# Kernel tuning notes

Measured on AMD Instinct MI355X. Metric: run time of the kernel, lower is better.

## Reference

```python
import jax, jax.numpy as jnp
import numpy as np

B, LQ, LK = 16, 256, 256
DQ = DK = DV = H = 256


def setup_inputs() -> dict:
    key = jax.random.key(0)
    ks = jax.random.split(key, 7)
    queries = jax.random.normal(ks[0], (B, LQ, DQ), dtype=jnp.float32)
    keys = jax.random.normal(ks[1], (B, LK, DK), dtype=jnp.float32)
    values = jax.random.normal(ks[2], (B, LK, DV), dtype=jnp.float32)
    valid_lens = jax.random.randint(ks[3], (B,), 1, LK + 1).astype(jnp.int32)
    W_q = jax.random.normal(ks[4], (DQ, H), dtype=jnp.float32) / np.sqrt(DQ)
    W_k = jax.random.normal(ks[5], (DK, H), dtype=jnp.float32) / np.sqrt(DK)
    w_v = jax.random.normal(ks[6], (H,), dtype=jnp.float32) / np.sqrt(H)
    return {"queries": queries, "keys": keys, "values": values,
            "valid_lens": valid_lens, "W_q": W_q, "W_k": W_k, "w_v": w_v}


def reference(queries, keys, values, valid_lens, W_q, W_k, w_v):
    # Project queries and keys to the hidden size (no bias)
    q = jnp.einsum('bqd,dh->bqh', queries, W_q)          # (B, Lq, H)
    k = jnp.einsum('bkd,dh->bkh', keys, W_k)             # (B, Lk, H)
    # Broadcast-add, tanh, then contract with w_v -> scores (B, Lq, Lk)
    features = jnp.tanh(q[:, :, None, :] + k[:, None, :, :])  # (B, Lq, Lk, H)
    scores = jnp.einsum('bqkh,h->bqk', features, w_v)
    # Masked softmax over last axis: positions >= valid_len get -1e6
    mask = jnp.arange(scores.shape[-1]) < valid_lens[:, None, None]  # (B,1,Lk) bcast
    scores = jnp.where(mask, scores, jnp.float32(-1e6))
    attn = jax.nn.softmax(scores, axis=-1)
    # Dropout is identity at inference (training=False)
    return jnp.einsum('bqk,bkv->bqv', attn, values)      # (B, Lq, Dv)
```

## Files before the change

kernel.cpp:

```cpp
#include <hip/hip_runtime.h>

using bf16x8 = __attribute__((ext_vector_type(8))) __bf16;
using f32x4  = __attribute__((ext_vector_type(4))) float;
using f32x2  = __attribute__((ext_vector_type(2))) float;
using us8    = __attribute__((ext_vector_type(8))) unsigned short;

#define TWO_LOG2E 2.8853900817779268f
#define LOG2E 1.4426950408889634f

__device__ __forceinline__ unsigned short f2bf(float x) {
  unsigned int u = __float_as_uint(x);
  u = (u + 0x7fffu + ((u >> 16) & 1u)) >> 16;
  return (unsigned short)u;
}
__device__ __forceinline__ float bf2f(unsigned short h) {
  return __uint_as_float(((unsigned int)h) << 16);
}

__global__ __launch_bounds__(256) void tcast_kernel(
    const float* __restrict__ Wq, const float* __restrict__ Wk,
    const float* __restrict__ vals, const float* __restrict__ wv,
    const int* __restrict__ vlens,
    unsigned short* __restrict__ wt_hi, unsigned short* __restrict__ wt_lo,
    unsigned short* __restrict__ vt_hi, unsigned short* __restrict__ vt_lo,
    float* __restrict__ wv2, float* __restrict__ Wsum,
    unsigned short* __restrict__ jobs, int* __restrict__ ctr) {
  if (blockIdx.x == 0) {
    int t = threadIdx.x;
    wv2[t] = -2.0f * wv[t];
    if (t < 64) {
      float s = wv[t] + wv[t + 64] + wv[t + 128] + wv[t + 192];
#pragma unroll
      for (int off = 1; off < 64; off <<= 1) s += __shfl_xor(s, off, 64);
      if (t == 0) Wsum[0] = s;
    }
    if (t == 0) {
      ctr[0] = 0;
      int n = 0;
      for (int lvl = 4; lvl >= 1; --lvl)
        for (int b = 0; b < 16; ++b) {
          int kt = (vlens[b] + 63) >> 6;
          if (kt == lvl)
            for (int q = 0; q < 32; ++q)
              jobs[n++] = (unsigned short)((b << 5) | q);
        }
    }
  }
  __shared__ float tile[32][33];
  int m = blockIdx.x >> 6;
  int ts = blockIdx.x & 63;
  int R0 = (ts >> 3) << 5, C0 = (ts & 7) << 5;
  const float* src = (m == 0) ? Wq : (m == 1) ? Wk : (vals + ((m - 2) << 16));
  int r = threadIdx.x >> 3, c4 = (threadIdx.x & 7) << 2;
  float4 v = *(const float4*)(src + (R0 + r) * 256 + C0 + c4);
  tile[r][c4] = v.x; tile[r][c4 + 1] = v.y; tile[r][c4 + 2] = v.z; tile[r][c4 + 3] = v.w;
  __syncthreads();
  float o0 = tile[c4 + 0][r], o1 = tile[c4 + 1][r];
  float o2 = tile[c4 + 2][r], o3 = tile[c4 + 3][r];
  unsigned short h0 = f2bf(o0), h1 = f2bf(o1), h2 = f2bf(o2), h3 = f2bf(o3);
  int base = ((m < 2) ? (m << 16) : ((m - 2) << 16)) + (C0 + r) * 256 + R0 + c4;
  unsigned short* dh = (m < 2) ? wt_hi : vt_hi;
  unsigned short* dl = (m < 2) ? wt_lo : vt_lo;
  *(ushort4*)(dh + base) = make_ushort4(h0, h1, h2, h3);
  *(ushort4*)(dl + base) = make_ushort4(f2bf(o0 - bf2f(h0)), f2bf(o1 - bf2f(h1)),
                                        f2bf(o2 - bf2f(h2)), f2bf(o3 - bf2f(h3)));
}

__global__ __launch_bounds__(256, 4) void proj_kernel(
    const float* __restrict__ q, const float* __restrict__ kk,
    const unsigned short* __restrict__ w_hi, const unsigned short* __restrict__ w_lo,
    const int* __restrict__ vlens, float* __restrict__ Rq, float* __restrict__ RkT) {
  int wave = threadIdx.x >> 6, lane = threadIdx.x & 63;
  int mt = (blockIdx.x << 1) + (wave & 1);
  int m0 = mt << 4;
  int g = mt >> 8;
  int r = lane & 15, qd = lane >> 4;
  int nbase = (blockIdx.y << 6) + ((wave >> 1) << 5);
  if (g) {
    int bb = (m0 >> 8) & 15;
    if ((m0 & 255) >= vlens[bb]) {
      f32x4 z = {0.f, 0.f, 0.f, 0.f};
      int kloc = (m0 & 255) + qd * 4;
#pragma unroll
      for (int tI = 0; tI < 2; ++tI)
        *(f32x4*)(RkT + (bb << 16) + (nbase + (tI << 4) + r) * 256 + kloc) = z;
      return;
    }
  }
  int row = m0 + r;
  const float* A = (g == 0) ? (q + row * 256) : (kk + (row - 4096) * 256);
  int boff0 = (g << 16) + (nbase + r) * 256 + qd * 8;
  int boff1 = boff0 + (16 << 8);
  f32x4 acc0 = {0.f, 0.f, 0.f, 0.f}, acc1 = {0.f, 0.f, 0.f, 0.f};
#pragma unroll
  for (int kh = 0; kh < 2; ++kh) {
    bf16x8 ah[4], al[4];
#pragma unroll
    for (int s = 0; s < 4; ++s) {
      const float* p = A + qd * 8 + (kh * 4 + s) * 32;
      float4 f0 = *(const float4*)p;
      float4 f1 = *(const float4*)(p + 4);
      float fv[8] = {f0.x, f0.y, f0.z, f0.w, f1.x, f1.y, f1.z, f1.w};
#pragma unroll
      for (int j = 0; j < 8; ++j) {
        __bf16 h = (__bf16)fv[j];
        ah[s][j] = h;
        al[s][j] = (__bf16)(fv[j] - (float)h);
      }
    }
#pragma unroll
    for (int s = 0; s < 4; ++s) {
      int off = (kh * 4 + s) * 32;
      bf16x8 bh0 = *(const bf16x8*)(w_hi + boff0 + off);
      bf16x8 bl0 = *(const bf16x8*)(w_lo + boff0 + off);
      acc0 = __builtin_amdgcn_mfma_f32_16x16x32_bf16(ah[s], bh0, acc0, 0, 0, 0);
      acc0 = __builtin_amdgcn_mfma_f32_16x16x32_bf16(ah[s], bl0, acc0, 0, 0, 0);
      acc0 = __builtin_amdgcn_mfma_f32_16x16x32_bf16(al[s], bh0, acc0, 0, 0, 0);
      bf16x8 bh1 = *(const bf16x8*)(w_hi + boff1 + off);
      bf16x8 bl1 = *(const bf16x8*)(w_lo + boff1 + off);
      acc1 = __builtin_amdgcn_mfma_f32_16x16x32_bf16(ah[s], bh1, acc1, 0, 0, 0);
      acc1 = __builtin_amdgcn_mfma_f32_16x16x32_bf16(ah[s], bl1, acc1, 0, 0, 0);
      acc1 = __builtin_amdgcn_mfma_f32_16x16x32_bf16(al[s], bh1, acc1, 0, 0, 0);
    }
  }
#pragma unroll
  for (int tI = 0; tI < 2; ++tI) {
    f32x4 acc = tI ? acc1 : acc0;
    int n0 = nbase + (tI << 4);
    f32x4 ex;
#pragma unroll
    for (int i = 0; i < 4; ++i) {
      float l = acc[i] * TWO_LOG2E;
      l = fminf(fmaxf(l, -27.f), 27.f);
      ex[i] = __builtin_amdgcn_exp2f(l);
    }
    if (g == 0) {
#pragma unroll
      for (int i = 0; i < 4; ++i)
        Rq[(m0 + qd * 4 + i) * 256 + n0 + r] = ex[i];
    } else {
      int b = (m0 >> 8) & 15;
      int kloc = (m0 & 255) + qd * 4;
      *(f32x4*)(RkT + (b << 16) + (n0 + r) * 256 + kloc) = ex;
    }
  }
}

__global__ __launch_bounds__(512) void sav3_kernel(
    const float* __restrict__ Rq, const float* __restrict__ RkT,
    const float* __restrict__ wv2, const float* __restrict__ Wsum,
    const int* __restrict__ vlens, const unsigned short* __restrict__ jobs,
    int* __restrict__ ctr,
    const unsigned short* __restrict__ vhi, const unsigned short* __restrict__ vlo,
    float* __restrict__ out) {
  __shared__ __align__(16) float kT[256 * 68];
  __shared__ __align__(16) float rqs[8 * 260];
  __shared__ __align__(16) float scs[8 * 260];
  __shared__ __align__(16) unsigned short athi[16 * 264];
  __shared__ float wv2s[256];
  __shared__ int s_item;
  const int t = threadIdx.x;
  const int w = t >> 6, lane = t & 63;
  const float wsum = Wsum[0];

  if (t < 256) wv2s[t] = wv2[t];
  for (int i = t; i < 8 * 264; i += 512) athi[8 * 264 + i] = 0;

  for (;;) {
    __syncthreads();
    if (t == 0) s_item = atomicAdd(ctr, 1);
    __syncthreads();
    const int jid = s_item;
    if (jid >= 512) return;
    const int jw = jobs[jid];
    const int b = jw >> 5, q0 = (jw & 31) << 3;
    const int qrow = (b << 8) + q0;
    const int vl = vlens[b];
    const int ktiles = (vl + 63) >> 6;

    {
      int row = t >> 6, c = lane << 2;
      *(float4*)(rqs + row * 260 + c) = *(const float4*)(Rq + (qrow + row) * 256 + c);
    }
    for (int kt = 0; kt < ktiles; ++kt) {
      const int k0 = kt << 6;
      __syncthreads();
      {
        int h0 = t >> 2, kc = (t & 3) << 4;
#pragma unroll
        for (int p = 0; p < 2; ++p) {
          int h = h0 + (p << 7);
          const float* gk = RkT + (b << 16) + h * 256 + k0 + kc;
          *(float4*)(kT + h * 68 + kc)      = *(const float4*)gk;
          *(float4*)(kT + h * 68 + kc + 4)  = *(const float4*)(gk + 4);
          *(float4*)(kT + h * 68 + kc + 8)  = *(const float4*)(gk + 8);
          *(float4*)(kT + h * 68 + kc + 12) = *(const float4*)(gk + 12);
        }
      }
      __syncthreads();
      float a = 0.f;
#pragma unroll 4
      for (int h = 0; h < 256; ++h) {
        float qa = rqs[w * 260 + h];
        float wm = wv2s[h];
        float rk = kT[h * 68 + lane];
        float d = __builtin_fmaf(rk, qa, 1.0f);
        a = __builtin_fmaf(__builtin_amdgcn_rcpf(d), wm, a);
      }
      scs[w * 260 + k0 + lane] = a + wsum;
    }
    __syncthreads();

    {
      int c0 = lane << 2;
      float4 x = *(const float4*)(scs + w * 260 + c0);
      float p[4] = {x.x, x.y, x.z, x.w};
#pragma unroll
      for (int i = 0; i < 4; ++i)
        if (c0 + i >= vl) p[i] = -1e6f;
      float mx = fmaxf(fmaxf(p[0], p[1]), fmaxf(p[2], p[3]));
#pragma unroll
      for (int off = 1; off < 64; off <<= 1) mx = fmaxf(mx, __shfl_xor(mx, off, 64));
      float sm = 0.f;
#pragma unroll
      for (int i = 0; i < 4; ++i) {
        p[i] = __builtin_amdgcn_exp2f((p[i] - mx) * LOG2E);
        sm += p[i];
      }
#pragma unroll
      for (int off = 1; off < 64; off <<= 1) sm += __shfl_xor(sm, off, 64);
      float rs = __builtin_amdgcn_rcpf(sm);
      ushort4 vh;
      vh.x = f2bf(p[0] * rs); vh.y = f2bf(p[1] * rs);
      vh.z = f2bf(p[2] * rs); vh.w = f2bf(p[3] * rs);
      *(ushort4*)(athi + w * 264 + c0) = vh;
    }
    __syncthreads();

    {
      const int r = lane & 15, qd = lane >> 4;
      const int smax = (vl + 31) >> 5;
      const int nb = w << 5;
      const int boff = (b << 16) + (nb + r) * 256 + qd * 8;
      f32x4 acc0 = {0.f, 0.f, 0.f, 0.f}, acc1 = {0.f, 0.f, 0.f, 0.f};
      for (int s = 0; s < smax; ++s) {
        bf16x8 pa = *(const bf16x8*)(athi + r * 264 + qd * 8 + s * 32);
        bf16x8 bh0 = *(const bf16x8*)(vhi + boff + s * 32);
        bf16x8 bl0 = *(const bf16x8*)(vlo + boff + s * 32);
        acc0 = __builtin_amdgcn_mfma_f32_16x16x32_bf16(pa, bh0, acc0, 0, 0, 0);
        acc0 = __builtin_amdgcn_mfma_f32_16x16x32_bf16(pa, bl0, acc0, 0, 0, 0);
        bf16x8 bh1 = *(const bf16x8*)(vhi + boff + (16 << 8) + s * 32);
        bf16x8 bl1 = *(const bf16x8*)(vlo + boff + (16 << 8) + s * 32);
        acc1 = __builtin_amdgcn_mfma_f32_16x16x32_bf16(pa, bh1, acc1, 0, 0, 0);
        acc1 = __builtin_amdgcn_mfma_f32_16x16x32_bf16(pa, bl1, acc1, 0, 0, 0);
      }
      if (qd < 2) {
#pragma unroll
        for (int i = 0; i < 4; ++i) {
          out[(b << 16) + (q0 + qd * 4 + i) * 256 + nb + r]      = acc0[i];
          out[(b << 16) + (q0 + qd * 4 + i) * 256 + nb + 16 + r] = acc1[i];
        }
      }
    }
  }
}

extern "C" void kernel_launch(void* const* d_in, const int* in_sizes, int n_in,
                              void* d_out, int out_size, void* d_ws, size_t ws_size,
                              hipStream_t stream) {
  const float* queries = (const float*)d_in[0];
  const float* keys    = (const float*)d_in[1];
  const float* values  = (const float*)d_in[2];
  const int*   vlens   = (const int*)d_in[3];
  const float* Wq      = (const float*)d_in[4];
  const float* Wk      = (const float*)d_in[5];
  const float* wv      = (const float*)d_in[6];
  float* out = (float*)d_out;
  char* ws = (char*)d_ws;

  unsigned short* wt_hi = (unsigned short*)(ws + 0);
  unsigned short* wt_lo = (unsigned short*)(ws + 262144);
  unsigned short* vt_hi = (unsigned short*)(ws + 524288);
  unsigned short* vt_lo = (unsigned short*)(ws + 2621440);
  float*          Rq    = (float*)(ws + 4718592);
  float*          RkT   = (float*)(ws + 8912896);
  float*          wv2   = (float*)(ws + 13107200);
  float*          Wsum  = (float*)(ws + 13108224);
  unsigned short* jobs  = (unsigned short*)(ws + 13109248);
  int*            ctr   = (int*)(ws + 13110272);

  tcast_kernel<<<1152, 256, 0, stream>>>(Wq, Wk, values, wv, vlens,
                                         wt_hi, wt_lo, vt_hi, vt_lo, wv2, Wsum,
                                         jobs, ctr);
  proj_kernel<<<dim3(256, 4), 256, 0, stream>>>(queries, keys, wt_hi, wt_lo,
                                                vlens, Rq, RkT);
  sav3_kernel<<<256, 512, 0, stream>>>(Rq, RkT, wv2, Wsum, vlens, jobs, ctr,
                                       vt_hi, vt_lo, out);
}
```

Before: 146.0 us.

## Stage 128-key mega-tiles and compute two query rows per wave in score loop

The score kernel now loads 128 keys of the exp-transformed key projection into shared memory per barrier instead of 64, halving the number of load/sync rounds. Each wave handles two query rows for one 64-key half, so each key value read from LDS is reused twice, and query and weight values are read as float4 vectors. The cost is a larger LDS footprint (about 135KB for kTm) and idle waves when the valid length leaves only one 64-key tile in the last mega-tile.

```diff
diff --git a/kernel.cpp b/kernel.cpp
--- a/kernel.cpp
+++ b/kernel.cpp
@@ -146,18 +146,18 @@
   }
 }
 
-__global__ __launch_bounds__(512) void sav3_kernel(
+__global__ __launch_bounds__(512) void sav5_kernel(
     const float* __restrict__ Rq, const float* __restrict__ RkT,
     const float* __restrict__ wv2, const float* __restrict__ Wsum,
     const int* __restrict__ vlens, const unsigned short* __restrict__ jobs,
     int* __restrict__ ctr,
     const unsigned short* __restrict__ vhi, const unsigned short* __restrict__ vlo,
     float* __restrict__ out) {
-  __shared__ __align__(16) float kT[256 * 68];
+  __shared__ __align__(16) float kTm[256 * 132];
   __shared__ __align__(16) float rqs[8 * 260];
-  __shared__ __align__(16) float scs[8 * 260];
+  __shared__ __align__(16) float scs[8 * 264];
   __shared__ __align__(16) unsigned short athi[16 * 264];
-  __shared__ float wv2s[256];
+  __shared__ __align__(16) float wv2s[256];
   __shared__ int s_item;
   const int t = threadIdx.x;
   const int w = t >> 6, lane = t & 63;
@@ -165,6 +165,10 @@
 
   if (t < 256) wv2s[t] = wv2[t];
   for (int i = t; i < 8 * 264; i += 512) athi[8 * 264 + i] = 0;
+
+  const int ql  = (w & 3) << 1;
+  const int ktl = w >> 2;
+  const int kloc = (ktl << 6) + lane;
 
   for (;;) {
     __syncthreads();
@@ -176,44 +180,60 @@
     const int b = jw >> 5, q0 = (jw & 31) << 3;
     const int qrow = (b << 8) + q0;
     const int vl = vlens[b];
-    const int ktiles = (vl + 63) >> 6;
+    const int kt64 = (vl + 63) >> 6;
+    const int nmega = (kt64 + 1) >> 1;
 
     {
       int row = t >> 6, c = lane << 2;
       *(float4*)(rqs + row * 260 + c) = *(const float4*)(Rq + (qrow + row) * 256 + c);
     }
-    for (int kt = 0; kt < ktiles; ++kt) {
-      const int k0 = kt << 6;
+
+    for (int m = 0; m < nmega; ++m) {
       __syncthreads();
       {
-        int h0 = t >> 2, kc = (t & 3) << 4;
-#pragma unroll
-        for (int p = 0; p < 2; ++p) {
-          int h = h0 + (p << 7);
-          const float* gk = RkT + (b << 16) + h * 256 + k0 + kc;
-          *(float4*)(kT + h * 68 + kc)      = *(const float4*)gk;
-          *(float4*)(kT + h * 68 + kc + 4)  = *(const float4*)(gk + 4);
-          *(float4*)(kT + h * 68 + kc + 8)  = *(const float4*)(gk + 8);
-          *(float4*)(kT + h * 68 + kc + 12) = *(const float4*)(gk + 12);
+        int hh = t >> 3, kc = (t & 7) << 4;
+#pragma unroll
+        for (int p = 0; p < 4; ++p) {
+          int h = (p << 6) + hh;
+          const float* gk = RkT + (b << 16) + h * 256 + (m << 7) + kc;
+          float* dst = kTm + h * 132 + kc;
+          *(float4*)(dst)      = *(const float4*)(gk);
+          *(float4*)(dst + 4)  = *(const float4*)(gk + 4);
+          *(float4*)(dst + 8)  = *(const float4*)(gk + 8);
+          *(float4*)(dst + 12) = *(const float4*)(gk + 12);
         }
       }
       __syncthreads();
-      float a = 0.f;
-#pragma unroll 4
-      for (int h = 0; h < 256; ++h) {
-        float qa = rqs[w * 260 + h];
-        float wm = wv2s[h];
-        float rk = kT[h * 68 + lane];
-        float d = __builtin_fmaf(rk, qa, 1.0f);
-        a = __builtin_fmaf(__builtin_amdgcn_rcpf(d), wm, a);
-      }
-      scs[w * 260 + k0 + lane] = a + wsum;
+      const int tiles = kt64 - (m << 1);
+      if (ktl < tiles) {
+        const float* kp = kTm + kloc;
+        const float* qa0 = rqs + ql * 260;
+        const float* qa1 = qa0 + 260;
+        float acc0 = 0.f, acc1 = 0.f;
+#pragma unroll 2
+        for (int h = 0; h < 256; h += 4) {
+          f32x4 wa = *(const f32x4*)(wv2s + h);
+          f32x4 a0 = *(const f32x4*)(qa0 + h);
+          f32x4 a1 = *(const f32x4*)(qa1 + h);
+#pragma unroll
+          for (int j = 0; j < 4; ++j) {
+            float rk = kp[(h + j) * 132];
+            float d0 = __builtin_fmaf(rk, a0[j], 1.0f);
+            float d1 = __builtin_fmaf(rk, a1[j], 1.0f);
+            acc0 = __builtin_fmaf(__builtin_amdgcn_rcpf(d0), wa[j], acc0);
+            acc1 = __builtin_fmaf(__builtin_amdgcn_rcpf(d1), wa[j], acc1);
+          }
+        }
+        const int kg = (m << 7) + kloc;
+        scs[ql * 264 + kg]       = acc0 + wsum;
+        scs[(ql + 1) * 264 + kg] = acc1 + wsum;
+      }
     }
     __syncthreads();
 
     {
       int c0 = lane << 2;
-      float4 x = *(const float4*)(scs + w * 260 + c0);
+      float4 x = *(const float4*)(scs + w * 264 + c0);
       float p[4] = {x.x, x.y, x.z, x.w};
 #pragma unroll
       for (int i = 0; i < 4; ++i)
@@ -294,6 +314,6 @@
                                          jobs, ctr);
   proj_kernel<<<dim3(256, 4), 256, 0, stream>>>(queries, keys, wt_hi, wt_lo,
                                                 vlens, Rq, RkT);
-  sav3_kernel<<<256, 512, 0, stream>>>(Rq, RkT, wv2, Wsum, vlens, jobs, ctr,
+  sav5_kernel<<<256, 512, 0, stream>>>(Rq, RkT, wv2, Wsum, vlens, jobs, ctr,
                                        vt_hi, vt_lo, out);
 }
```

After: 147.0 us. Within noise of the previous version (+0.7%).

## Store key projection row-major and split H across half-waves in score kernel

Applied to the files above, without the earlier changes.

The projection kernel now writes the exponentiated key projection row-major (k, h) instead of transposed. The score kernel tiles keys in 32-row chunks with a padded LDS stride. Each half-wave covers half of the hidden dimension with float4 reads and the two halves are combined by a cross-lane shuffle. Query rows and w_v are read straight from global memory instead of being staged in LDS. This cuts LDS use, finer key tiling trims wasted work past valid_len, and the grid doubles to 512 persistent blocks, at the cost of redundant global/L1 reads of the query rows and an extra shuffle per tile.

```diff
diff --git a/kernel.cpp b/kernel.cpp
--- a/kernel.cpp
+++ b/kernel.cpp
@@ -69,7 +69,7 @@
 __global__ __launch_bounds__(256, 4) void proj_kernel(
     const float* __restrict__ q, const float* __restrict__ kk,
     const unsigned short* __restrict__ w_hi, const unsigned short* __restrict__ w_lo,
-    const int* __restrict__ vlens, float* __restrict__ Rq, float* __restrict__ RkT) {
+    const int* __restrict__ vlens, float* __restrict__ Rq, float* __restrict__ Rk) {
   int wave = threadIdx.x >> 6, lane = threadIdx.x & 63;
   int mt = (blockIdx.x << 1) + (wave & 1);
   int m0 = mt << 4;
@@ -80,10 +80,10 @@
     int bb = (m0 >> 8) & 15;
     if ((m0 & 255) >= vlens[bb]) {
       f32x4 z = {0.f, 0.f, 0.f, 0.f};
-      int kloc = (m0 & 255) + qd * 4;
-#pragma unroll
-      for (int tI = 0; tI < 2; ++tI)
-        *(f32x4*)(RkT + (bb << 16) + (nbase + (tI << 4) + r) * 256 + kloc) = z;
+      int krow = m0 - 4096;
+#pragma unroll
+      for (int c = 0; c < 2; ++c)
+        *(f32x4*)(Rk + (krow + r) * 256 + nbase + qd * 8 + c * 4) = z;
       return;
     }
   }
@@ -139,32 +139,32 @@
       for (int i = 0; i < 4; ++i)
         Rq[(m0 + qd * 4 + i) * 256 + n0 + r] = ex[i];
     } else {
-      int b = (m0 >> 8) & 15;
-      int kloc = (m0 & 255) + qd * 4;
-      *(f32x4*)(RkT + (b << 16) + (n0 + r) * 256 + kloc) = ex;
-    }
-  }
-}
-
-__global__ __launch_bounds__(512) void sav3_kernel(
-    const float* __restrict__ Rq, const float* __restrict__ RkT,
+#pragma unroll
+      for (int i = 0; i < 4; ++i)
+        Rk[((m0 - 4096) + qd * 4 + i) * 256 + n0 + r] = ex[i];
+    }
+  }
+}
+
+__global__ __launch_bounds__(512) void sav6_kernel(
+    const float* __restrict__ Rq, const float* __restrict__ Rk,
     const float* __restrict__ wv2, const float* __restrict__ Wsum,
     const int* __restrict__ vlens, const unsigned short* __restrict__ jobs,
     int* __restrict__ ctr,
     const unsigned short* __restrict__ vhi, const unsigned short* __restrict__ vlo,
     float* __restrict__ out) {
-  __shared__ __align__(16) float kT[256 * 68];
-  __shared__ __align__(16) float rqs[8 * 260];
+  __shared__ __align__(16) float kS[32 * 257];
   __shared__ __align__(16) float scs[8 * 260];
   __shared__ __align__(16) unsigned short athi[16 * 264];
-  __shared__ float wv2s[256];
   __shared__ int s_item;
   const int t = threadIdx.x;
   const int w = t >> 6, lane = t & 63;
   const float wsum = Wsum[0];
 
-  if (t < 256) wv2s[t] = wv2[t];
   for (int i = t; i < 8 * 264; i += 512) athi[8 * 264 + i] = 0;
+
+  const int skrow = t & 31, schunk = t >> 5;
+  const int ck = lane & 31, chg = lane >> 5;
 
   for (;;) {
     __syncthreads();
@@ -176,38 +176,38 @@
     const int b = jw >> 5, q0 = (jw & 31) << 3;
     const int qrow = (b << 8) + q0;
     const int vl = vlens[b];
-    const int ktiles = (vl + 63) >> 6;
-
-    {
-      int row = t >> 6, c = lane << 2;
-      *(float4*)(rqs + row * 260 + c) = *(const float4*)(Rq + (qrow + row) * 256 + c);
-    }
-    for (int kt = 0; kt < ktiles; ++kt) {
-      const int k0 = kt << 6;
+    const int kt32 = (vl + 31) >> 5;
+
+    const float* qp = Rq + (qrow + w) * 256 + (chg << 7);
+    const float* wp = wv2 + (chg << 7);
+
+    for (int kt = 0; kt < kt32; ++kt) {
+      const int k0 = kt << 5;
       __syncthreads();
       {
-        int h0 = t >> 2, kc = (t & 3) << 4;
-#pragma unroll
-        for (int p = 0; p < 2; ++p) {
-          int h = h0 + (p << 7);
-          const float* gk = RkT + (b << 16) + h * 256 + k0 + kc;
-          *(float4*)(kT + h * 68 + kc)      = *(const float4*)gk;
-          *(float4*)(kT + h * 68 + kc + 4)  = *(const float4*)(gk + 4);
-          *(float4*)(kT + h * 68 + kc + 8)  = *(const float4*)(gk + 8);
-          *(float4*)(kT + h * 68 + kc + 12) = *(const float4*)(gk + 12);
+        const float* gk = Rk + ((b << 8) + k0 + skrow) * 256 + (schunk << 4);
+        float* dst = kS + skrow * 257 + (schunk << 4);
+        *(float4*)(dst)      = *(const float4*)(gk);
+        *(float4*)(dst + 4)  = *(const float4*)(gk + 4);
+        *(float4*)(dst + 8)  = *(const float4*)(gk + 8);
+        *(float4*)(dst + 12) = *(const float4*)(gk + 12);
+      }
+      __syncthreads();
+      float acc = 0.f;
+      const float* kp = kS + ck * 257 + (chg << 7);
+#pragma unroll 4
+      for (int h = 0; h < 128; h += 4) {
+        f32x4 rk = *(const f32x4*)(kp + h);
+        f32x4 qa = *(const f32x4*)(qp + h);
+        f32x4 wa = *(const f32x4*)(wp + h);
+#pragma unroll
+        for (int j = 0; j < 4; ++j) {
+          float d = __builtin_fmaf(rk[j], qa[j], 1.0f);
+          acc = __builtin_fmaf(__builtin_amdgcn_rcpf(d), wa[j], acc);
         }
       }
-      __syncthreads();
-      float a = 0.f;
-#pragma unroll 4
-      for (int h = 0; h < 256; ++h) {
-        float qa = rqs[w * 260 + h];
-        float wm = wv2s[h];
-        float rk = kT[h * 68 + lane];
-        float d = __builtin_fmaf(rk, qa, 1.0f);
-        a = __builtin_fmaf(__builtin_amdgcn_rcpf(d), wm, a);
-      }
-      scs[w * 260 + k0 + lane] = a + wsum;
+      acc += __shfl_xor(acc, 32, 64);
+      if (lane < 32) scs[w * 260 + k0 + ck] = acc + wsum;
     }
     __syncthreads();
 
@@ -283,7 +283,7 @@
   unsigned short* vt_hi = (unsigned short*)(ws + 524288);
   unsigned short* vt_lo = (unsigned short*)(ws + 2621440);
   float*          Rq    = (float*)(ws + 4718592);
-  float*          RkT   = (float*)(ws + 8912896);
+  float*          Rk    = (float*)(ws + 8912896);
   float*          wv2   = (float*)(ws + 13107200);
   float*          Wsum  = (float*)(ws + 13108224);
   unsigned short* jobs  = (unsigned short*)(ws + 13109248);
@@ -293,7 +293,7 @@
                                          wt_hi, wt_lo, vt_hi, vt_lo, wv2, Wsum,
                                          jobs, ctr);
   proj_kernel<<<dim3(256, 4), 256, 0, stream>>>(queries, keys, wt_hi, wt_lo,
-                                                vlens, Rq, RkT);
-  sav3_kernel<<<256, 512, 0, stream>>>(Rq, RkT, wv2, Wsum, vlens, jobs, ctr,
+                                                vlens, Rq, Rk);
+  sav6_kernel<<<512, 512, 0, stream>>>(Rq, Rk, wv2, Wsum, vlens, jobs, ctr,
                                        vt_hi, vt_lo, out);
 }
```

New measurement: 211.3 us. 44.7% more time.
